# Kernel optimization log

Measured on AMD Instinct MI355X. Metric: run time of the kernel, lower is better.

Reference implementation:

```python
import jax, jax.numpy as jnp
import numpy as np

B, N, E, H = 4, 512, 512, 8   # batch, tokens, embedding_channels (=KV_size_S), num_heads
C = 4 * E                      # KV_size_C
D = E // H                     # head dim
EPS = 1e-5                     # InstanceNorm2d default eps


def _inorm(x, axes):
    # InstanceNorm2d (affine=False): normalize over spatial axes with biased variance
    m = jnp.mean(x, axis=axes, keepdims=True)
    v = jnp.var(x, axis=axes, keepdims=True)
    return (x - m) * jax.lax.rsqrt(v + EPS)


def setup_inputs() -> dict:
    key = jax.random.key(0)
    ks = jax.random.split(key, 24)
    s = 0.02
    inp = {
        'emb1': jax.random.normal(ks[0], (B, N, E), jnp.float32),
        'emb2': jax.random.normal(ks[1], (B, N, E), jnp.float32),
        'emb3': jax.random.normal(ks[2], (B, N, E), jnp.float32),
        'emb4': jax.random.normal(ks[3], (B, N, E), jnp.float32),
        'emb_C': jax.random.normal(ks[4], (B, N, C), jnp.float32),
        'Wq1': jax.random.normal(ks[5], (E, E), jnp.float32) * s,
        'Wq2': jax.random.normal(ks[6], (E, E), jnp.float32) * s,
        'Wq3': jax.random.normal(ks[7], (E, E), jnp.float32) * s,
        'Wq4': jax.random.normal(ks[8], (E, E), jnp.float32) * s,
        'Wk': jax.random.normal(ks[9], (E, E), jnp.float32) * s,
        'Wv': jax.random.normal(ks[10], (E, E), jnp.float32) * s,
        'WqC': jax.random.normal(ks[11], (C, C), jnp.float32) * s,
        'WkC': jax.random.normal(ks[12], (C, C), jnp.float32) * s,
        'WvC': jax.random.normal(ks[13], (C, C), jnp.float32) * s,
        'Wo1': jax.random.normal(ks[14], (E, E), jnp.float32) * s,
        'Wo2': jax.random.normal(ks[15], (E, E), jnp.float32) * s,
        'Wo3': jax.random.normal(ks[16], (E, E), jnp.float32) * s,
        'Wo4': jax.random.normal(ks[17], (E, E), jnp.float32) * s,
    }
    return inp


def _heads(x):
    # [B, N, E] -> [B, H, N, D]
    b, n, _ = x.shape
    return x.reshape(b, n, H, D).transpose(0, 2, 1, 3)


def reference(emb1, emb2, emb3, emb4, emb_C,
              Wq1, Wq2, Wq3, Wq4, Wk, Wv, WqC, WkC, WvC,
              Wo1, Wo2, Wo3, Wo4):
    # ---- channel cross-attention ----
    QC = emb_C @ WqC.T            # [B, N, C]
    KC = emb_C @ WkC.T
    VC = emb_C @ WvC.T
    attn_c = jnp.einsum('bnc,bnd->bcd', QC, KC)        # [B, C, C]
    sim_c = jax.nn.softmax(_inorm(attn_c, (1, 2)), axis=-1)  # psi1 + softmax(dim=3)
    ctx_c = jnp.einsum('bcd,bnd->bcn', sim_c, VC)      # [B, C, N]
    T_hat = ctx_c.transpose(0, 2, 1)                   # [B, N, C]
    # split last dim into 4 chunks of E, concat along tokens -> [B, 4N, E]
    KV_S = jnp.concatenate(jnp.split(T_hat, 4, axis=2), axis=1)

    # ---- spatial multi-head cross-attention, shared K/V ----
    K = _heads(KV_S @ Wk.T)       # [B, H, 4N, D]
    V = _heads(KV_S @ Wv.T)

    outs = []
    for emb, Wq, Wo in ((emb1, Wq1, Wo1), (emb2, Wq2, Wo2),
                        (emb3, Wq3, Wo3), (emb4, Wq4, Wo4)):
        Q = _heads(emb @ Wq.T)                          # [B, H, N, D]
        attn = jnp.einsum('bhnd,bhmd->bhnm', Q, K)      # [B, H, N, 4N]
        sim = jax.nn.softmax(_inorm(attn, (2, 3)), axis=-1)  # psi2 + softmax
        ctx = jnp.einsum('bhnm,bhmd->bhnd', sim, V)     # [B, H, N, D]
        ctx = ctx.transpose(0, 2, 1, 3).reshape(emb.shape[0], emb.shape[1], E)
        outs.append(ctx @ Wo.T)
    return tuple(outs)
```

## Files before the change

### kernel.cpp

```cpp
#include <hip/hip_runtime.h>
#include <hip/hip_bf16.h>
#include <hip/hip_fp16.h>

typedef long long i64;
typedef unsigned int u32;
typedef __attribute__((ext_vector_type(8))) short bf16x8;
typedef __attribute__((ext_vector_type(4))) float f32x4;

#define MFMA_BF16 __builtin_amdgcn_mfma_f32_16x16x32_bf16
#define VMCNT(n)  asm volatile("s_waitcnt vmcnt(" #n ")" ::: "memory")
#define LGKM0     asm volatile("s_waitcnt lgkmcnt(0)" ::: "memory")
#define SBAR      __builtin_amdgcn_s_barrier()
#define SCHED0    __builtin_amdgcn_sched_barrier(0)

__device__ __forceinline__ void glds16(const void* g, void* l){
    __builtin_amdgcn_global_load_lds((const __attribute__((address_space(1))) u32*)g,
                                     (__attribute__((address_space(3))) u32*)l, 16, 0, 0);
}
__device__ __forceinline__ void split1(float x, ushort& h, ushort& l){
    unsigned b = __float_as_uint(x);
    h = (ushort)(b >> 16);
    float hf = __uint_as_float(b & 0xFFFF0000u);
    float lf = x - hf;
    l = (ushort)(__float_as_uint(lf) >> 16);
}
__device__ __forceinline__ float bfpair(ushort h, ushort l){
    return __uint_as_float((u32)h << 16) + __uint_as_float((u32)l << 16);
}
__device__ __forceinline__ bf16x8 fragS(const ushort* P, int row, int g){
    return *(const bf16x8*)&P[row*64 + (((g) ^ (row & 7)) << 3)];
}

struct P4 { const void* p[4]; };
struct I4 { int v[4]; };

struct PSJobs { const float* s[13]; ushort* d[13]; int st[14]; };
__global__ __launch_bounds__(256) void presplit(PSJobs J){
    int bid = blockIdx.x, j = 0;
    while (bid >= J.st[j+1]) ++j;
    i64 base = (i64)(bid - J.st[j])*2048 + threadIdx.x*8;
    i64 loOff = (i64)(J.st[j+1] - J.st[j])*2048;
    const float* sp = J.s[j]; ushort* dp = J.d[j];
    float4 a = *(const float4*)&sp[base];
    float4 b = *(const float4*)&sp[base+4];
    float v[8] = {a.x,a.y,a.z,a.w,b.x,b.y,b.z,b.w};
    ushort h[8], l[8];
    #pragma unroll
    for (int t = 0; t < 8; ++t) split1(v[t], h[t], l[t]);
    *(ushort4*)&dp[base]         = make_ushort4(h[0],h[1],h[2],h[3]);
    *(ushort4*)&dp[base+4]       = make_ushort4(h[4],h[5],h[6],h[7]);
    *(ushort4*)&dp[loOff+base]   = make_ushort4(l[0],l[1],l[2],l[3]);
    *(ushort4*)&dp[loOff+base+4] = make_ushort4(l[4],l[5],l[6],l[7]);
}

template<int OUT>
__global__ __launch_bounds__(256) void gemm_ps(
    P4 Ap, P4 Bp, P4 Cp, I4 cmode, float* __restrict__ stats,
    int K, int zdiv,
    i64 ab2, i64 alda, i64 aLo,
    i64 bb2, i64 bldb, i64 bLo,
    i64 cb2, i64 cld, i64 cLo)
{
    __shared__ ushort Ah[2][4096], Al[2][4096], Bh[2][4096], Bl[2][4096];
    __shared__ float sred[4], qred[4];
    const int z = blockIdx.z, z1 = z / zdiv, z2 = z % zdiv;
    const int m0 = blockIdx.y*128, n0 = blockIdx.x*128;
    const int tid = threadIdx.x, lane = tid & 63, wid = tid >> 6;
    const int wm = wid >> 1, wn = wid & 1, fr = lane & 15, kc = lane >> 4;
    const ushort* Aps = (const ushort*)Ap.p[z1] + (i64)z2*ab2 + (i64)m0*alda;
    const ushort* Bps = (const ushort*)Bp.p[z1] + (i64)z2*bb2 + (i64)n0*bldb;

    const int srow = wid*32 + (lane >> 2);
    const int sg   = lane & 3;

    auto stageAB = [&](int k0, int pb){
        #pragma unroll
        for (int q = 0; q < 2; ++q) {
            int r  = srow + q*16;
            int gs = sg ^ ((r >> 1) & 3);
            const ushort* sa = Aps + (i64)r*alda + k0 + gs*8;
            glds16(sa,       &Ah[pb][(wid*32+q*16)*32]);
            glds16(sa + aLo, &Al[pb][(wid*32+q*16)*32]);
            const ushort* sb = Bps + (i64)r*bldb + k0 + gs*8;
            glds16(sb,       &Bh[pb][(wid*32+q*16)*32]);
            glds16(sb + bLo, &Bl[pb][(wid*32+q*16)*32]);
        }
    };
    auto rd = [&](const ushort* P, int row, int kcc)->bf16x8 {
        return *(const bf16x8*)&P[row*32 + ((kcc ^ ((row >> 1) & 3)) << 3)];
    };

    f32x4 acc[4][4];
    #pragma unroll
    for (int i = 0; i < 4; ++i)
        #pragma unroll
        for (int j = 0; j < 4; ++j) acc[i][j] = (f32x4){0.f,0.f,0.f,0.f};

    const int NT = K >> 5;
    stageAB(0, 0); stageAB(32, 1);

    for (int t = 0; t < NT; ++t) {
        const int cur = t & 1;
        if (t + 1 < NT) { VMCNT(8); } else { VMCNT(0); }
        SBAR;
        bf16x8 a_h[4], a_l[4], b_h[4], b_l[4];
        #pragma unroll
        for (int i = 0; i < 4; ++i) {
            int row = wm*64 + i*16 + fr;
            a_h[i] = rd(Ah[cur], row, kc);
            a_l[i] = rd(Al[cur], row, kc);
        }
        #pragma unroll
        for (int j = 0; j < 4; ++j) {
            int row = wn*64 + j*16 + fr;
            b_h[j] = rd(Bh[cur], row, kc);
            b_l[j] = rd(Bl[cur], row, kc);
        }
        __builtin_amdgcn_s_setprio(1);
        #pragma unroll
        for (int i = 0; i < 4; ++i)
            #pragma unroll
            for (int j = 0; j < 4; ++j) {
                acc[i][j] = MFMA_BF16(a_h[i], b_h[j], acc[i][j], 0, 0, 0);
                acc[i][j] = MFMA_BF16(a_h[i], b_l[j], acc[i][j], 0, 0, 0);
                acc[i][j] = MFMA_BF16(a_l[i], b_h[j], acc[i][j], 0, 0, 0);
            }
        __builtin_amdgcn_s_setprio(0);
        LGKM0;
        SBAR;
        SCHED0;
        if (t + 2 < NT) stageAB((t+2) << 5, cur);
    }

    const i64 cbase = (i64)z2*cb2;
    if (OUT == 0) {
        float* C = (float*)Cp.p[z1];
        #pragma unroll
        for (int i = 0; i < 4; ++i)
            #pragma unroll
            for (int j = 0; j < 4; ++j)
                #pragma unroll
                for (int r = 0; r < 4; ++r) {
                    int m = m0 + wm*64 + i*16 + kc*4 + r;
                    int n = n0 + wn*64 + j*16 + fr;
                    C[cbase + (i64)m*cld + n] = acc[i][j][r];
                }
    } else if (OUT == 1) {
        ushort* C = (ushort*)Cp.p[z1];
        const int cfg = cmode.v[z1];
        const int tr = cfg >> 30;
        const i64 ldv = cfg & 0x3FFFFFFF;
        #pragma unroll
        for (int i = 0; i < 4; ++i)
            #pragma unroll
            for (int j = 0; j < 4; ++j)
                #pragma unroll
                for (int r = 0; r < 4; ++r) {
                    int m = m0 + wm*64 + i*16 + kc*4 + r;
                    int n = n0 + wn*64 + j*16 + fr;
                    ushort h, l; split1(acc[i][j][r], h, l);
                    i64 off = cbase + (tr ? (i64)n*ldv + m : (i64)m*ldv + n);
                    C[off] = h; C[off + cLo] = l;
                }
    } else if (OUT == 2) {
        __half* C = (__half*)Cp.p[z1];
        float ls = 0.f, lq = 0.f;
        #pragma unroll
        for (int i = 0; i < 4; ++i)
            #pragma unroll
            for (int j = 0; j < 4; ++j)
                #pragma unroll
                for (int r = 0; r < 4; ++r) {
                    int m = m0 + wm*64 + i*16 + kc*4 + r;
                    int n = n0 + wn*64 + j*16 + fr;
                    float v = acc[i][j][r];
                    ls += v; lq += v*v;
                    C[cbase + (i64)m*cld + n] = __float2half(v);
                }
        #pragma unroll
        for (int off = 32; off; off >>= 1) { ls += __shfl_xor(ls, off); lq += __shfl_xor(lq, off); }
        if (lane == 0) { sred[wid] = ls; qred[wid] = lq; }
        __syncthreads();
        if (tid == 0) {
            atomicAdd(&stats[2*z],   sred[0]+sred[1]+sred[2]+sred[3]);
            atomicAdd(&stats[2*z+1], qred[0]+qred[1]+qred[2]+qred[3]);
        }
    } else {
        ushort* C = (ushort*)Cp.p[z1];
        #pragma unroll
        for (int i = 0; i < 4; ++i)
            #pragma unroll
            for (int j = 0; j < 4; ++j)
                #pragma unroll
                for (int r = 0; r < 4; ++r) {
                    int m = m0 + wm*64 + i*16 + kc*4 + r;
                    int n = n0 + wn*64 + j*16 + fr;
                    ushort h, l; split1(acc[i][j][r], h, l);
                    i64 off = cbase + ((i64)(m >> 9) << 18) + ((i64)n << 9) + (m & 511);
                    C[off] = h; C[off + cLo] = l;
                }
    }
}

__global__ __launch_bounds__(256) void softmax_rows(
    __half* __restrict__ attn, ushort* __restrict__ lo,
    const float* __restrict__ stats, int rows_per_stat, float inv_count)
{
    const int ROWLEN = 2048;
    const int row = blockIdx.x;
    const int sidx = row / rows_per_stat;
    float sm = stats[2*sidx], sq = stats[2*sidx+1];
    float mean = sm * inv_count;
    float var = fmaxf(sq * inv_count - mean*mean, 0.f);
    float scale = rsqrtf(var + 1e-5f);
    __half* rp = attn + (i64)row * ROWLEN;
    ushort* hp = (ushort*)rp;
    ushort* lp = lo + (i64)row * ROWLEN;
    const int tid = threadIdx.x;
    float v[8]; float mx = -3.4e38f;
    #pragma unroll
    for (int s = 0; s < 8; ++s) { float x = __half2float(rp[tid + s*256]) * scale; v[s] = x; mx = fmaxf(mx, x); }
    #pragma unroll
    for (int off = 32; off; off >>= 1) mx = fmaxf(mx, __shfl_xor(mx, off));
    __shared__ float red[4];
    if ((tid & 63) == 0) red[tid >> 6] = mx;
    __syncthreads();
    mx = fmaxf(fmaxf(red[0], red[1]), fmaxf(red[2], red[3]));
    float ls = 0.f;
    #pragma unroll
    for (int s = 0; s < 8; ++s) { float e = __expf(v[s] - mx); v[s] = e; ls += e; }
    #pragma unroll
    for (int off = 32; off; off >>= 1) ls += __shfl_xor(ls, off);
    __syncthreads();
    if ((tid & 63) == 0) red[tid >> 6] = ls;
    __syncthreads();
    float inv = 1.f / (red[0] + red[1] + red[2] + red[3]);
    #pragma unroll
    for (int s = 0; s < 8; ++s) {
        ushort h, l; split1(v[s] * inv, h, l);
        hp[tid + s*256] = h; lp[tid + s*256] = l;
    }
}

__global__ __launch_bounds__(256) void gram64(
    const ushort* __restrict__ hi, i64 loOff, float* __restrict__ parts,
    i64 bstride, i64 zs2)
{
    __shared__ float T[16][68];
    __shared__ float csred[4][64];
    const int z = blockIdx.x;
    const int tid = threadIdx.x;
    const ushort* base = hi + (i64)(z>>3)*bstride + (i64)blockIdx.z*zs2
                       + (i64)blockIdx.y*256*512 + (z&7)*64;
    float g[4][4] = {{0.f}};
    float cs = 0.f;
    const int sr = tid >> 4, sc = (tid & 15) * 4;
    const int col = tid & 63, qq = tid >> 6;
    for (int grp = 0; grp < 16; ++grp) {
        i64 idx = (i64)(grp*16 + sr)*512 + sc;
        ushort4 hv = *(const ushort4*)&base[idx];
        ushort4 lv = *(const ushort4*)&base[loOff + idx];
        float4 ld;
        ld.x = bfpair(hv.x, lv.x); ld.y = bfpair(hv.y, lv.y);
        ld.z = bfpair(hv.z, lv.z); ld.w = bfpair(hv.w, lv.w);
        __syncthreads();
        *(float4*)&T[sr][sc] = ld;
        __syncthreads();
        #pragma unroll
        for (int rr = 0; rr < 16; ++rr) {
            const float4 a = *(const float4*)&T[rr][sr*4];
            const float4 b = *(const float4*)&T[rr][sc];
            g[0][0]+=a.x*b.x; g[0][1]+=a.x*b.y; g[0][2]+=a.x*b.z; g[0][3]+=a.x*b.w;
            g[1][0]+=a.y*b.x; g[1][1]+=a.y*b.y; g[1][2]+=a.y*b.z; g[1][3]+=a.y*b.w;
            g[2][0]+=a.z*b.x; g[2][1]+=a.z*b.y; g[2][2]+=a.z*b.z; g[2][3]+=a.z*b.w;
            g[3][0]+=a.w*b.x; g[3][1]+=a.w*b.y; g[3][2]+=a.w*b.z; g[3][3]+=a.w*b.w;
        }
        cs += T[qq*4+0][col] + T[qq*4+1][col] + T[qq*4+2][col] + T[qq*4+3][col];
    }
    float* outp = parts + (i64)((blockIdx.z*gridDim.y + blockIdx.y)*gridDim.x + blockIdx.x)*4160;
    #pragma unroll
    for (int x = 0; x < 4; ++x)
        #pragma unroll
        for (int y = 0; y < 4; ++y)
            outp[(sr*4+x)*64 + sc + y] = g[x][y];
    csred[qq][col] = cs;
    __syncthreads();
    if (tid < 64) outp[4096 + tid] = csred[0][tid]+csred[1][tid]+csred[2][tid]+csred[3][tid];
}

__global__ __launch_bounds__(256) void fin_stats(
    const float* __restrict__ gq, const float* __restrict__ gk,
    float* __restrict__ ss)
{
    const int z = blockIdx.x, s = blockIdx.y;
    const int tid = threadIdx.x;
    const int lane = tid & 63, wid = tid >> 6;
    const float* q0 = gq + (i64)((s*2+0)*32 + z)*4160;
    const float* q1 = gq + (i64)((s*2+1)*32 + z)*4160;
    float p2 = 0.f;
    for (int i = tid; i < 4096; i += 256) {
        float a = q0[i] + q1[i];
        float b = 0.f;
        #pragma unroll
        for (int c = 0; c < 8; ++c) b += gk[(i64)(c*32 + z)*4160 + i];
        p2 += a*b;
    }
    float p1 = 0.f;
    if (tid < 64) {
        float a = q0[4096+tid] + q1[4096+tid];
        float b = 0.f;
        #pragma unroll
        for (int c = 0; c < 8; ++c) b += gk[(i64)(c*32 + z)*4160 + 4096 + tid];
        p1 = a*b;
    }
    #pragma unroll
    for (int off = 32; off; off >>= 1) { p2 += __shfl_xor(p2, off); p1 += __shfl_xor(p1, off); }
    __shared__ float r2[4], r1[4];
    if (lane == 0) { r2[wid] = p2; r1[wid] = p1; }
    __syncthreads();
    if (tid == 0) {
        float S2 = r2[0]+r2[1]+r2[2]+r2[3];
        float S1 = r1[0]+r1[1]+r1[2]+r1[3];
        const float inv = 1.f/1048576.f;
        float mu = S1*inv;
        float var = fmaxf(S2*inv - mu*mu, 0.f);
        float sc = rsqrtf(var + 1e-5f);
        ss[(s*32+z)*2] = sc;
        ss[(s*32+z)*2+1] = sc*mu;
    }
}

__global__ __launch_bounds__(256) void flash_ps(
    const ushort* __restrict__ Qp, const ushort* __restrict__ Kp,
    const ushort* __restrict__ Vtp, const float* __restrict__ ss,
    ushort* __restrict__ ctxp)
{
    __shared__ ushort QPh[4096], QPl[4096];
    __shared__ ushort Kh[2][4096], Kl[2][4096];
    __shared__ ushort Vh[2][4096], Vl[2][4096];
    const int qt = blockIdx.x, zz = blockIdx.y, s = blockIdx.z;
    const int b = zz >> 3, hD = (zz & 7) * 64;
    const float scale = ss[(s*32+zz)*2], shift = ss[(s*32+zz)*2+1];
    const ushort* Qb = Qp + (i64)s*2097152 + (i64)b*262144 + (i64)(qt*64)*512 + hD;
    const ushort* Kb = Kp + (i64)b*1048576 + hD;
    const ushort* Vb = Vtp + (i64)b*1048576 + (i64)hD*2048;
    const int tid = threadIdx.x, lane = tid & 63, wid = tid >> 6;
    const int wq = wid >> 1, wk = wid & 1, fr = lane & 15, kc = lane >> 4;

    auto stage64 = [&](const ushort* src, i64 ld, i64 lo, ushort* Lh, ushort* Ll){
        #pragma unroll
        for (int q = 0; q < 2; ++q) {
            int rb = wid*16 + q*8;
            int r = rb + (lane >> 3);
            int gs = (lane & 7) ^ (r & 7);
            const ushort* p = src + (i64)r*ld + gs*8;
            glds16(p,      &Lh[rb*64]);
            glds16(p + lo, &Ll[rb*64]);
        }
    };

    stage64(Qb, 512, 1048576, QPh, QPl);
    stage64(Kb, 512, 4194304, Kh[0], Kl[0]);
    stage64(Vb, 2048, 4194304, Vh[0], Vl[0]);
    VMCNT(8); SBAR;
    bf16x8 qh[2][2], ql[2][2];
    #pragma unroll
    for (int i = 0; i < 2; ++i)
        #pragma unroll
        for (int ks = 0; ks < 2; ++ks) {
            int row = wq*32 + i*16 + fr;
            qh[i][ks] = fragS(QPh, row, ks*4 + kc);
            ql[i][ks] = fragS(QPl, row, ks*4 + kc);
        }
    LGKM0; SBAR;
    SCHED0;
    stage64(Kb + (i64)64*512, 512, 4194304, Kh[1], Kl[1]);
    stage64(Vb + 64, 2048, 4194304, Vh[1], Vl[1]);

    f32x4 ctx[2][2];
    #pragma unroll
    for (int i = 0; i < 2; ++i)
        #pragma unroll
        for (int j = 0; j < 2; ++j) ctx[i][j] = (f32x4){0.f,0.f,0.f,0.f};
    float den_lr[2][4] = {{0.f}};

    for (int t = 0; t < 32; ++t) {
        const int cur = t & 1;
        if (t < 31) { VMCNT(8); } else { VMCNT(0); }
        SBAR;
        f32x4 sacc[2][2];
        #pragma unroll
        for (int i = 0; i < 2; ++i)
            #pragma unroll
            for (int j = 0; j < 2; ++j) sacc[i][j] = (f32x4){0.f,0.f,0.f,0.f};
        #pragma unroll
        for (int ks = 0; ks < 2; ++ks) {
            bf16x8 khf[2], klf[2];
            #pragma unroll
            for (int j = 0; j < 2; ++j) {
                int row = wk*32 + j*16 + fr;
                khf[j] = fragS(Kh[cur], row, ks*4 + kc);
                klf[j] = fragS(Kl[cur], row, ks*4 + kc);
            }
            __builtin_amdgcn_s_setprio(1);
            #pragma unroll
            for (int i = 0; i < 2; ++i)
                #pragma unroll
                for (int j = 0; j < 2; ++j) {
                    sacc[i][j] = MFMA_BF16(qh[i][ks], khf[j], sacc[i][j], 0, 0, 0);
                    sacc[i][j] = MFMA_BF16(qh[i][ks], klf[j], sacc[i][j], 0, 0, 0);
                    sacc[i][j] = MFMA_BF16(ql[i][ks], khf[j], sacc[i][j], 0, 0, 0);
                }
            __builtin_amdgcn_s_setprio(0);
        }
        #pragma unroll
        for (int i = 0; i < 2; ++i)
            #pragma unroll
            for (int j = 0; j < 2; ++j)
                #pragma unroll
                for (int r = 0; r < 4; ++r) {
                    float p = __expf(sacc[i][j][r]*scale - shift);
                    den_lr[i][r] += p;
                    ushort h, l; split1(p, h, l);
                    int row = wq*32 + i*16 + kc*4 + r;
                    int col = wk*32 + j*16 + fr;
                    int pos = row*64 + ((((col>>3) ^ (row&7)) << 3) | (col & 7));
                    QPh[pos] = h; QPl[pos] = l;
                }
        LGKM0; SBAR;
        SCHED0;
        if (t < 30) stage64(Kb + (i64)((t+2)*64)*512, 512, 4194304, Kh[cur], Kl[cur]);
        #pragma unroll
        for (int ks = 0; ks < 2; ++ks) {
            bf16x8 vhf[2], vlf[2], pah[2], pal[2];
            #pragma unroll
            for (int j = 0; j < 2; ++j) {
                int row = wk*32 + j*16 + fr;
                vhf[j] = fragS(Vh[cur], row, ks*4 + kc);
                vlf[j] = fragS(Vl[cur], row, ks*4 + kc);
            }
            #pragma unroll
            for (int i = 0; i < 2; ++i) {
                int row = wq*32 + i*16 + fr;
                pah[i] = fragS(QPh, row, ks*4 + kc);
                pal[i] = fragS(QPl, row, ks*4 + kc);
            }
            __builtin_amdgcn_s_setprio(1);
            #pragma unroll
            for (int i = 0; i < 2; ++i)
                #pragma unroll
                for (int j = 0; j < 2; ++j) {
                    ctx[i][j] = MFMA_BF16(pah[i], vhf[j], ctx[i][j], 0, 0, 0);
                    ctx[i][j] = MFMA_BF16(pah[i], vlf[j], ctx[i][j], 0, 0, 0);
                    ctx[i][j] = MFMA_BF16(pal[i], vhf[j], ctx[i][j], 0, 0, 0);
                }
            __builtin_amdgcn_s_setprio(0);
        }
        LGKM0; SBAR;
        SCHED0;
        if (t < 30) stage64(Vb + (t+2)*64, 2048, 4194304, Vh[cur], Vl[cur]);
    }

    float* denf = (float*)QPl;
    #pragma unroll
    for (int i = 0; i < 2; ++i)
        #pragma unroll
        for (int r = 0; r < 4; ++r) {
            float d = den_lr[i][r];
            d += __shfl_xor(d, 1); d += __shfl_xor(d, 2);
            d += __shfl_xor(d, 4); d += __shfl_xor(d, 8);
            if (fr == 0) denf[wk*64 + wq*32 + i*16 + kc*4 + r] = d;
        }
    __syncthreads();
    ushort* Cb = ctxp + (i64)s*2097152 + (i64)b*262144;
    #pragma unroll
    for (int i = 0; i < 2; ++i)
        #pragma unroll
        for (int j = 0; j < 2; ++j)
            #pragma unroll
            for (int r = 0; r < 4; ++r) {
                int row = wq*32 + i*16 + kc*4 + r;
                int col = wk*32 + j*16 + fr;
                float dv = denf[row] + denf[64 + row];
                ushort h, l; split1(ctx[i][j][r] / dv, h, l);
                i64 off = (i64)(qt*64 + row)*512 + hD + col;
                Cb[off] = h; Cb[off + 1048576] = l;
            }
}

static inline P4 p4x(const void* a, const void* b, const void* c, const void* d){
    P4 x; x.p[0]=a; x.p[1]=b; x.p[2]=c; x.p[3]=d; return x;
}
static inline P4 p4x(const void* a){ return p4x(a,a,a,a); }
static inline I4 i4x(int a, int b, int c, int d){ I4 x; x.v[0]=a; x.v[1]=b; x.v[2]=c; x.v[3]=d; return x; }
#define TRC(ld) ((1<<30)|(ld))

extern "C" void kernel_launch(void* const* d_in, const int* in_sizes, int n_in,
                              void* d_out, int out_size, void* d_ws, size_t ws_size,
                              hipStream_t stream)
{
    (void)in_sizes; (void)n_in; (void)out_size;
    const float* emb[4] = {(const float*)d_in[0], (const float*)d_in[1],
                           (const float*)d_in[2], (const float*)d_in[3]};
    const float* embC = (const float*)d_in[4];
    const float* Wq[4] = {(const float*)d_in[5], (const float*)d_in[6],
                          (const float*)d_in[7], (const float*)d_in[8]};
    const float* Wk  = (const float*)d_in[9];
    const float* Wv  = (const float*)d_in[10];
    const float* WqC = (const float*)d_in[11];
    const float* WkC = (const float*)d_in[12];
    const float* WvC = (const float*)d_in[13];
    const float* Wo[4] = {(const float*)d_in[14], (const float*)d_in[15],
                          (const float*)d_in[16], (const float*)d_in[17]};
    float* out = (float*)d_out;

    char* ws = (char*)d_ws;
    const size_t MB = 1024*1024;
    if (ws_size < 128*MB + 512) return;
    auto U = [&](size_t mb){ return (ushort*)(ws + mb*MB); };
    float* stats = (float*)(ws + 122*MB);
    float* ssbuf = (float*)(ws + 122*MB + 1024);
    float* GKp   = (float*)(ws + 48*MB);
    float* GQp   = (float*)(ws + 53*MB);
    __half* scores = (__half*)(ws + 16*MB);

    hipMemsetAsync(stats, 0, 512, stream);

    {
        PSJobs J;
        const float* srcs[13] = {embC, WqC, WkC, WvC, Wk, Wv,
                                 Wq[0],Wq[1],Wq[2],Wq[3], Wo[0],Wo[1],Wo[2]};
        ushort* dsts[13] = {U(0),U(16),U(32),U(48),U(64),U(65),
                            U(66),U(67),U(68),U(69), U(70),U(71),U(72)};
        int blks[13] = {2048,2048,2048,2048,128,128, 128,128,128,128, 128,128,128};
        int a = 0;
        for (int j = 0; j < 13; ++j) { J.s[j]=srcs[j]; J.d[j]=dsts[j]; J.st[j]=a; a+=blks[j]; }
        J.st[13] = a;
        presplit<<<dim3(a), 256, 0, stream>>>(J);
    }
    gemm_ps<1><<<dim3(16, 4, 12), 256, 0, stream>>>(
        p4x(U(0)), p4x(U(16), U(32), U(48), U(48)), p4x(U(74), U(90), U(106), U(106)),
        i4x(TRC(512), TRC(512), 2048, 2048), nullptr, 2048, 4,
        1048576, 2048, 4194304,   0, 2048, 4194304,   1048576, 0, 4194304);
    {
        PSJobs J;
        const float* srcs[13] = {emb[0], emb[1], emb[2], emb[3], Wo[3],
                                 nullptr,nullptr,nullptr,nullptr,nullptr,nullptr,nullptr,nullptr};
        ushort* dsts[13] = {U(0), U(4), U(8), U(12), U(73),
                            nullptr,nullptr,nullptr,nullptr,nullptr,nullptr,nullptr,nullptr};
        int blks[5] = {512,512,512,512,128};
        int a = 0;
        for (int j = 0; j < 5; ++j) { J.s[j]=srcs[j]; J.d[j]=dsts[j]; J.st[j]=a; a+=blks[j]; }
        for (int j = 5; j < 14; ++j) J.st[j] = a;
        presplit<<<dim3(a), 256, 0, stream>>>(J);
    }
    gemm_ps<2><<<dim3(16, 16, 4), 256, 0, stream>>>(
        p4x(U(74)), p4x(U(90)), p4x(scores), i4x(0,0,0,0), stats, 512, 4,
        1048576, 512, 4194304,   1048576, 512, 4194304,   4194304, 2048, 0);
    softmax_rows<<<dim3(4*2048), 256, 0, stream>>>(scores, U(74), stats, 2048, 1.f/4194304.f);
    gemm_ps<3><<<dim3(4, 16, 4), 256, 0, stream>>>(
        p4x(U(16)), p4x(U(106)), p4x(U(48)), i4x(0,0,0,0), nullptr, 2048, 4,
        4194304, 2048, 30408704,   1048576, 2048, 4194304,   1048576, 0, 4194304);
    gemm_ps<1><<<dim3(4, 16, 8), 256, 0, stream>>>(
        p4x(U(48)), p4x(U(64), U(65), U(65), U(65)), p4x(U(74), U(90), U(90), U(90)),
        i4x(512, TRC(2048), 0, 0), nullptr, 512, 4,
        1048576, 512, 4194304,   0, 512, 262144,   1048576, 0, 4194304);
    gemm_ps<1><<<dim3(4, 4, 16), 256, 0, stream>>>(
        p4x(U(0), U(4), U(8), U(12)), p4x(U(66), U(67), U(68), U(69)),
        p4x(U(106), U(110), U(114), U(118)),
        i4x(512,512,512,512), nullptr, 512, 4,
        262144, 512, 1048576,   0, 512, 262144,   262144, 0, 1048576);
    gram64<<<dim3(32, 8, 1), 256, 0, stream>>>(U(74), 4194304, GKp, 1048576, 0);
    gram64<<<dim3(32, 2, 4), 256, 0, stream>>>(U(106), 1048576, GQp, 262144, 2097152);
    fin_stats<<<dim3(32, 4), 256, 0, stream>>>(GQp, GKp, ssbuf);
    flash_ps<<<dim3(8, 32, 4), 256, 0, stream>>>(U(106), U(74), U(90), ssbuf, U(16));
    gemm_ps<0><<<dim3(4, 4, 16), 256, 0, stream>>>(
        p4x(U(16), U(20), U(24), U(28)), p4x(U(70), U(71), U(72), U(73)),
        p4x(out, out + 1048576, out + 2097152, out + 3145728),
        i4x(0,0,0,0), nullptr, 512, 4,
        262144, 512, 1048576,   0, 512, 262144,   262144, 512, 1048576);
}
```

Before: 672.7 us.

## Enlarge GEMM tiles to 256x256 with 512 threads and XCD-aware block remap

The split-bf16 GEMM moves from 128x128 tiles with 256 threads to 256x256 tiles with 512 threads (8 waves, each computing 128x64). It also uses a flattened 1D grid whose block index is permuted across the 8 XCDs, with a configurable inner batch grouping. Larger tiles halve the global/LDS traffic per FLOP, and the remap is meant to improve L2 locality. The costs are 128KB of LDS per block, far fewer blocks (as few as 64 on a 256-CU part, so under-occupancy), and heavier accumulator register pressure.

```diff
diff --git a/kernel.cpp b/kernel.cpp
--- a/kernel.cpp
+++ b/kernel.cpp
@@ -54,45 +54,51 @@
 }
 
 template<int OUT>
-__global__ __launch_bounds__(256) void gemm_ps(
+__global__ __launch_bounds__(512, 2) void gemm_big(
     P4 Ap, P4 Bp, P4 Cp, I4 cmode, float* __restrict__ stats,
-    int K, int zdiv,
+    int K, int zdiv, int ci, int Y, int X,
     i64 ab2, i64 alda, i64 aLo,
     i64 bb2, i64 bldb, i64 bLo,
     i64 cb2, i64 cld, i64 cLo)
 {
-    __shared__ ushort Ah[2][4096], Al[2][4096], Bh[2][4096], Bl[2][4096];
-    __shared__ float sred[4], qred[4];
-    const int z = blockIdx.z, z1 = z / zdiv, z2 = z % zdiv;
-    const int m0 = blockIdx.y*128, n0 = blockIdx.x*128;
+    __shared__ ushort Ah[2][8192], Al[2][8192], Bh[2][8192], Bl[2][8192];
+    __shared__ float sred[8], qred[8];
+    const int q8 = gridDim.x >> 3;
+    int wg = (blockIdx.x & 7) * q8 + (blockIdx.x >> 3);
+    const int z2i = wg % ci; wg /= ci;
+    const int y = wg % Y;    wg /= Y;
+    const int x = wg % X;
+    const int zo = wg / X;
+    const int z = zo*ci + z2i;
+    const int z1 = z / zdiv, z2 = z % zdiv;
+    const int m0 = y*256, n0 = x*256;
+
     const int tid = threadIdx.x, lane = tid & 63, wid = tid >> 6;
-    const int wm = wid >> 1, wn = wid & 1, fr = lane & 15, kc = lane >> 4;
+    const int wm = wid >> 2, wn = wid & 3, fr = lane & 15, kc = lane >> 4;
     const ushort* Aps = (const ushort*)Ap.p[z1] + (i64)z2*ab2 + (i64)m0*alda;
     const ushort* Bps = (const ushort*)Bp.p[z1] + (i64)z2*bb2 + (i64)n0*bldb;
 
-    const int srow = wid*32 + (lane >> 2);
-    const int sg   = lane & 3;
-
     auto stageAB = [&](int k0, int pb){
         #pragma unroll
-        for (int q = 0; q < 2; ++q) {
-            int r  = srow + q*16;
-            int gs = sg ^ ((r >> 1) & 3);
+        for (int qq = 0; qq < 2; ++qq) {
+            int rb = qq*128 + wid*16;
+            int r  = rb + (lane >> 2);
+            int gs = (lane & 3) ^ ((r >> 1) & 3);
             const ushort* sa = Aps + (i64)r*alda + k0 + gs*8;
-            glds16(sa,       &Ah[pb][(wid*32+q*16)*32]);
-            glds16(sa + aLo, &Al[pb][(wid*32+q*16)*32]);
+            glds16(sa,       &Ah[pb][rb*32]);
+            glds16(sa + aLo, &Al[pb][rb*32]);
             const ushort* sb = Bps + (i64)r*bldb + k0 + gs*8;
-            glds16(sb,       &Bh[pb][(wid*32+q*16)*32]);
-            glds16(sb + bLo, &Bl[pb][(wid*32+q*16)*32]);
+            glds16(sb,       &Bh[pb][rb*32]);
+            glds16(sb + bLo, &Bl[pb][rb*32]);
         }
     };
     auto rd = [&](const ushort* P, int row, int kcc)->bf16x8 {
         return *(const bf16x8*)&P[row*32 + ((kcc ^ ((row >> 1) & 3)) << 3)];
     };
 
-    f32x4 acc[4][4];
-    #pragma unroll
-    for (int i = 0; i < 4; ++i)
+    f32x4 acc[8][4];
+    #pragma unroll
+    for (int i = 0; i < 8; ++i)
         #pragma unroll
         for (int j = 0; j < 4; ++j) acc[i][j] = (f32x4){0.f,0.f,0.f,0.f};
 
@@ -103,29 +109,33 @@
         const int cur = t & 1;
         if (t + 1 < NT) { VMCNT(8); } else { VMCNT(0); }
         SBAR;
-        bf16x8 a_h[4], a_l[4], b_h[4], b_l[4];
-        #pragma unroll
-        for (int i = 0; i < 4; ++i) {
-            int row = wm*64 + i*16 + fr;
-            a_h[i] = rd(Ah[cur], row, kc);
-            a_l[i] = rd(Al[cur], row, kc);
-        }
+        bf16x8 b_h[4], b_l[4];
         #pragma unroll
         for (int j = 0; j < 4; ++j) {
             int row = wn*64 + j*16 + fr;
             b_h[j] = rd(Bh[cur], row, kc);
             b_l[j] = rd(Bl[cur], row, kc);
         }
-        __builtin_amdgcn_s_setprio(1);
-        #pragma unroll
-        for (int i = 0; i < 4; ++i)
-            #pragma unroll
-            for (int j = 0; j < 4; ++j) {
-                acc[i][j] = MFMA_BF16(a_h[i], b_h[j], acc[i][j], 0, 0, 0);
-                acc[i][j] = MFMA_BF16(a_h[i], b_l[j], acc[i][j], 0, 0, 0);
-                acc[i][j] = MFMA_BF16(a_l[i], b_h[j], acc[i][j], 0, 0, 0);
+        #pragma unroll
+        for (int half = 0; half < 2; ++half) {
+            bf16x8 a_h[4], a_l[4];
+            #pragma unroll
+            for (int ii = 0; ii < 4; ++ii) {
+                int row = wm*128 + (half*4 + ii)*16 + fr;
+                a_h[ii] = rd(Ah[cur], row, kc);
+                a_l[ii] = rd(Al[cur], row, kc);
             }
-        __builtin_amdgcn_s_setprio(0);
+            __builtin_amdgcn_s_setprio(1);
+            #pragma unroll
+            for (int ii = 0; ii < 4; ++ii)
+                #pragma unroll
+                for (int j = 0; j < 4; ++j) {
+                    acc[half*4+ii][j] = MFMA_BF16(a_h[ii], b_h[j], acc[half*4+ii][j], 0, 0, 0);
+                    acc[half*4+ii][j] = MFMA_BF16(a_h[ii], b_l[j], acc[half*4+ii][j], 0, 0, 0);
+                    acc[half*4+ii][j] = MFMA_BF16(a_l[ii], b_h[j], acc[half*4+ii][j], 0, 0, 0);
+                }
+            __builtin_amdgcn_s_setprio(0);
+        }
         LGKM0;
         SBAR;
         SCHED0;
@@ -136,12 +146,12 @@
     if (OUT == 0) {
         float* C = (float*)Cp.p[z1];
         #pragma unroll
-        for (int i = 0; i < 4; ++i)
+        for (int i = 0; i < 8; ++i)
             #pragma unroll
             for (int j = 0; j < 4; ++j)
                 #pragma unroll
                 for (int r = 0; r < 4; ++r) {
-                    int m = m0 + wm*64 + i*16 + kc*4 + r;
+                    int m = m0 + wm*128 + i*16 + kc*4 + r;
                     int n = n0 + wn*64 + j*16 + fr;
                     C[cbase + (i64)m*cld + n] = acc[i][j][r];
                 }
@@ -151,12 +161,12 @@
         const int tr = cfg >> 30;
         const i64 ldv = cfg & 0x3FFFFFFF;
         #pragma unroll
-        for (int i = 0; i < 4; ++i)
+        for (int i = 0; i < 8; ++i)
             #pragma unroll
             for (int j = 0; j < 4; ++j)
                 #pragma unroll
                 for (int r = 0; r < 4; ++r) {
-                    int m = m0 + wm*64 + i*16 + kc*4 + r;
+                    int m = m0 + wm*128 + i*16 + kc*4 + r;
                     int n = n0 + wn*64 + j*16 + fr;
                     ushort h, l; split1(acc[i][j][r], h, l);
                     i64 off = cbase + (tr ? (i64)n*ldv + m : (i64)m*ldv + n);
@@ -166,12 +176,12 @@
         __half* C = (__half*)Cp.p[z1];
         float ls = 0.f, lq = 0.f;
         #pragma unroll
-        for (int i = 0; i < 4; ++i)
+        for (int i = 0; i < 8; ++i)
             #pragma unroll
             for (int j = 0; j < 4; ++j)
                 #pragma unroll
                 for (int r = 0; r < 4; ++r) {
-                    int m = m0 + wm*64 + i*16 + kc*4 + r;
+                    int m = m0 + wm*128 + i*16 + kc*4 + r;
                     int n = n0 + wn*64 + j*16 + fr;
                     float v = acc[i][j][r];
                     ls += v; lq += v*v;
@@ -182,18 +192,21 @@
         if (lane == 0) { sred[wid] = ls; qred[wid] = lq; }
         __syncthreads();
         if (tid == 0) {
-            atomicAdd(&stats[2*z],   sred[0]+sred[1]+sred[2]+sred[3]);
-            atomicAdd(&stats[2*z+1], qred[0]+qred[1]+qred[2]+qred[3]);
+            float s = 0.f, qq = 0.f;
+            #pragma unroll
+            for (int w = 0; w < 8; ++w) { s += sred[w]; qq += qred[w]; }
+            atomicAdd(&stats[2*z],   s);
+            atomicAdd(&stats[2*z+1], qq);
         }
     } else {
         ushort* C = (ushort*)Cp.p[z1];
         #pragma unroll
-        for (int i = 0; i < 4; ++i)
+        for (int i = 0; i < 8; ++i)
             #pragma unroll
             for (int j = 0; j < 4; ++j)
                 #pragma unroll
                 for (int r = 0; r < 4; ++r) {
-                    int m = m0 + wm*64 + i*16 + kc*4 + r;
+                    int m = m0 + wm*128 + i*16 + kc*4 + r;
                     int n = n0 + wn*64 + j*16 + fr;
                     ushort h, l; split1(acc[i][j][r], h, l);
                     i64 off = cbase + ((i64)(m >> 9) << 18) + ((i64)n << 9) + (m & 511);
@@ -279,10 +292,10 @@
     }
     float* outp = parts + (i64)((blockIdx.z*gridDim.y + blockIdx.y)*gridDim.x + blockIdx.x)*4160;
     #pragma unroll
-    for (int x = 0; x < 4; ++x)
-        #pragma unroll
-        for (int y = 0; y < 4; ++y)
-            outp[(sr*4+x)*64 + sc + y] = g[x][y];
+    for (int xx = 0; xx < 4; ++xx)
+        #pragma unroll
+        for (int yy = 0; yy < 4; ++yy)
+            outp[(sr*4+xx)*64 + sc + yy] = g[xx][yy];
     csred[qq][col] = cs;
     __syncthreads();
     if (tid < 64) outp[4096 + tid] = csred[0][tid]+csred[1][tid]+csred[2][tid]+csred[3][tid];
@@ -538,9 +551,10 @@
         J.st[13] = a;
         presplit<<<dim3(a), 256, 0, stream>>>(J);
     }
-    gemm_ps<1><<<dim3(16, 4, 12), 256, 0, stream>>>(
+    gemm_big<1><<<dim3(192), 512, 0, stream>>>(
         p4x(U(0)), p4x(U(16), U(32), U(48), U(48)), p4x(U(74), U(90), U(106), U(106)),
-        i4x(TRC(512), TRC(512), 2048, 2048), nullptr, 2048, 4,
+        i4x(TRC(512), TRC(512), 2048, 2048), nullptr,
+        2048, 4, 4, 2, 8,
         1048576, 2048, 4194304,   0, 2048, 4194304,   1048576, 0, 4194304);
     {
         PSJobs J;
@@ -554,29 +568,34 @@
         for (int j = 5; j < 14; ++j) J.st[j] = a;
         presplit<<<dim3(a), 256, 0, stream>>>(J);
     }
-    gemm_ps<2><<<dim3(16, 16, 4), 256, 0, stream>>>(
-        p4x(U(74)), p4x(U(90)), p4x(scores), i4x(0,0,0,0), stats, 512, 4,
+    gemm_big<2><<<dim3(256), 512, 0, stream>>>(
+        p4x(U(74)), p4x(U(90)), p4x(scores), i4x(0,0,0,0), stats,
+        512, 4, 1, 8, 8,
         1048576, 512, 4194304,   1048576, 512, 4194304,   4194304, 2048, 0);
     softmax_rows<<<dim3(4*2048), 256, 0, stream>>>(scores, U(74), stats, 2048, 1.f/4194304.f);
-    gemm_ps<3><<<dim3(4, 16, 4), 256, 0, stream>>>(
-        p4x(U(16)), p4x(U(106)), p4x(U(48)), i4x(0,0,0,0), nullptr, 2048, 4,
+    gemm_big<3><<<dim3(64), 512, 0, stream>>>(
+        p4x(U(16)), p4x(U(106)), p4x(U(48)), i4x(0,0,0,0), nullptr,
+        2048, 4, 1, 8, 2,
         4194304, 2048, 30408704,   1048576, 2048, 4194304,   1048576, 0, 4194304);
-    gemm_ps<1><<<dim3(4, 16, 8), 256, 0, stream>>>(
+    gemm_big<1><<<dim3(128), 512, 0, stream>>>(
         p4x(U(48)), p4x(U(64), U(65), U(65), U(65)), p4x(U(74), U(90), U(90), U(90)),
-        i4x(512, TRC(2048), 0, 0), nullptr, 512, 4,
+        i4x(512, TRC(2048), 0, 0), nullptr,
+        512, 4, 4, 8, 2,
         1048576, 512, 4194304,   0, 512, 262144,   1048576, 0, 4194304);
-    gemm_ps<1><<<dim3(4, 4, 16), 256, 0, stream>>>(
+    gemm_big<1><<<dim3(64), 512, 0, stream>>>(
         p4x(U(0), U(4), U(8), U(12)), p4x(U(66), U(67), U(68), U(69)),
         p4x(U(106), U(110), U(114), U(118)),
-        i4x(512,512,512,512), nullptr, 512, 4,
+        i4x(512,512,512,512), nullptr,
+        512, 4, 4, 2, 2,
         262144, 512, 1048576,   0, 512, 262144,   262144, 0, 1048576);
     gram64<<<dim3(32, 8, 1), 256, 0, stream>>>(U(74), 4194304, GKp, 1048576, 0);
     gram64<<<dim3(32, 2, 4), 256, 0, stream>>>(U(106), 1048576, GQp, 262144, 2097152);
     fin_stats<<<dim3(32, 4), 256, 0, stream>>>(GQp, GKp, ssbuf);
     flash_ps<<<dim3(8, 32, 4), 256, 0, stream>>>(U(106), U(74), U(90), ssbuf, U(16));
-    gemm_ps<0><<<dim3(4, 4, 16), 256, 0, stream>>>(
+    gemm_big<0><<<dim3(64), 512, 0, stream>>>(
         p4x(U(16), U(20), U(24), U(28)), p4x(U(70), U(71), U(72), U(73)),
         p4x(out, out + 1048576, out + 2097152, out + 3145728),
-        i4x(0,0,0,0), nullptr, 512, 4,
+        i4x(0,0,0,0), nullptr,
+        512, 4, 4, 2, 2,
         262144, 512, 1048576,   0, 512, 262144,   262144, 512, 1048576);
 }
```

Result: slower. 878.0 us (+30.5%).
